# Performance work log

Measured on AMD Instinct MI355X. Metric: run time of the kernel, lower is better.

The kernel has to match this reference:

```python
import jax, jax.numpy as jnp
import numpy as np

DIM = 128
N_VARS = 2048
N_CLAUSES = 8192
N_ROUNDS = 26
ADJ_DENSITY = 0.0015  # ~6 literals per clause


def setup_inputs() -> dict:
    key = jax.random.key(0)
    ks = iter(jax.random.split(key, 40))

    def w(shape):
        fan_in = shape[-1]
        return jax.random.normal(next(ks), shape, jnp.float32) / jnp.sqrt(jnp.float32(fan_in))

    def b(shape):
        return jax.random.normal(next(ks), shape, jnp.float32) * 0.05

    adj = (jax.random.uniform(next(ks), (2 * N_VARS, N_CLAUSES)) < ADJ_DENSITY).astype(jnp.float32)
    inp = {
        'adj': adj,
        'l_init_w': w((DIM, 1)), 'l_init_b': b((DIM,)),
        'c_init_w': w((DIM, 1)), 'c_init_b': b((DIM,)),
        'lmsg_w1': w((DIM, DIM)), 'lmsg_b1': b((DIM,)),
        'lmsg_w2': w((DIM, DIM)), 'lmsg_b2': b((DIM,)),
        'lmsg_w3': w((DIM, DIM)), 'lmsg_b3': b((DIM,)),
        'cmsg_w1': w((DIM, DIM)), 'cmsg_b1': b((DIM,)),
        'cmsg_w2': w((DIM, DIM)), 'cmsg_b2': b((DIM,)),
        'cmsg_w3': w((DIM, DIM)), 'cmsg_b3': b((DIM,)),
        'l_wih': w((4 * DIM, 2 * DIM)), 'l_whh': w((4 * DIM, DIM)),
        'l_bih': b((4 * DIM,)), 'l_bhh': b((4 * DIM,)),
        'c_wih': w((4 * DIM, DIM)), 'c_whh': w((4 * DIM, DIM)),
        'c_bih': b((4 * DIM,)), 'c_bhh': b((4 * DIM,)),
        'lvote_w1': w((DIM, DIM)), 'lvote_b1': b((DIM,)),
        'lvote_w2': w((DIM, DIM)), 'lvote_b2': b((DIM,)),
        'lvote_w3': w((1, DIM)), 'lvote_b3': b((1,)),
    }
    return inp


def _mlp(x, w1, b1, w2, b2, w3, b3):
    x = jax.nn.relu(x @ w1.T + b1)
    x = jax.nn.relu(x @ w2.T + b2)
    return x @ w3.T + b3


def _lstm_step(x, h, c, wih, whh, bih, bhh):
    # torch.nn.LSTM gate order: i, f, g, o
    g = x @ wih.T + h @ whh.T + bih + bhh
    i, f, gg, o = jnp.split(g, 4, axis=-1)
    c = jax.nn.sigmoid(f) * c + jax.nn.sigmoid(i) * jnp.tanh(gg)
    h = jax.nn.sigmoid(o) * jnp.tanh(c)
    return h, c


def reference(adj, l_init_w, l_init_b, c_init_w, c_init_b,
              lmsg_w1, lmsg_b1, lmsg_w2, lmsg_b2, lmsg_w3, lmsg_b3,
              cmsg_w1, cmsg_b1, cmsg_w2, cmsg_b2, cmsg_w3, cmsg_b3,
              l_wih, l_whh, l_bih, l_bhh,
              c_wih, c_whh, c_bih, c_bhh,
              lvote_w1, lvote_b1, lvote_w2, lvote_b2, lvote_w3, lvote_b3):
    n_lits, n_clauses = adj.shape
    n_vars = n_lits // 2
    dim = l_init_b.shape[0]

    # L_init / C_init: Linear(1,dim) applied to ones(1), tiled across rows
    Lh = jnp.broadcast_to(l_init_w[:, 0] + l_init_b, (n_lits, dim))
    Ch = jnp.broadcast_to(c_init_w[:, 0] + c_init_b, (n_clauses, dim))
    Lc = jnp.zeros((n_lits, dim), jnp.float32)
    Cc = jnp.zeros((n_clauses, dim), jnp.float32)

    def step(carry, _):
        Lh, Lc, Ch, Cc = carry
        L_pre = _mlp(Lh, lmsg_w1, lmsg_b1, lmsg_w2, lmsg_b2, lmsg_w3, lmsg_b3)
        LC_msg = adj.T @ L_pre                       # [n_clauses, dim]
        Ch, Cc = _lstm_step(LC_msg, Ch, Cc, c_wih, c_whh, c_bih, c_bhh)
        C_pre = _mlp(Ch, cmsg_w1, cmsg_b1, cmsg_w2, cmsg_b2, cmsg_w3, cmsg_b3)
        CL_msg = adj @ C_pre                         # [2*n_vars, dim]
        L_flip = jnp.concatenate([Lh[n_vars:], Lh[:n_vars]], axis=0)
        x = jnp.concatenate([CL_msg, L_flip], axis=1)  # [2*n_vars, 2*dim]
        Lh, Lc = _lstm_step(x, Lh, Lc, l_wih, l_whh, l_bih, l_bhh)
        return (Lh, Lc, Ch, Cc), None

    (Lh, Lc, Ch, Cc), _ = jax.lax.scan(step, (Lh, Lc, Ch, Cc), None, length=N_ROUNDS)

    logits = Lh
    vote = _mlp(logits, lvote_w1, lvote_b1, lvote_w2, lvote_b2, lvote_w3, lvote_b3)  # [2*n_vars, 1]
    vote_join = jnp.concatenate([vote[:n_vars], vote[n_vars:]], axis=1)  # [n_vars, 2]
    vote_mean = jnp.mean(vote_join)[None]  # single problem in batch -> [1]
    return vote_mean, vote, logits
```

## Files before the change

### kernel.cpp

```cpp
#include <hip/hip_runtime.h>
#include <math.h>

#define NL 4096
#define NV 2048
#define NC 8192
#define DIM 128
#define NG 512
#define NROUNDS 26

#define CSEG 32
#define CSEGLEN 128
#define CSEGCAP 12
#define LSEG 32
#define LSEGLEN 256
#define LSEGCAP 16
#define CCAP 32
#define LCAP 48

__device__ __forceinline__ float sigf(float x){ return 1.0f/(1.0f+expf(-x)); }

__global__ void k_transpose(const float* __restrict__ src, float* __restrict__ dst,
                            int R, int C){
  __shared__ float t[32][33];
  int cb = blockIdx.x*32, rb = blockIdx.y*32;
  int x = threadIdx.x, y = threadIdx.y;
  for (int i = y; i < 32; i += 8){
    int r = rb+i, c = cb+x;
    if (r < R && c < C) t[i][x] = src[(size_t)r*C + c];
  }
  __syncthreads();
  for (int i = y; i < 32; i += 8){
    int c = cb+i, r = rb+x;
    if (c < C && r < R) dst[(size_t)c*R + r] = t[x][i];
  }
}

__global__ void k_permq(const float* __restrict__ W, int K,
                        float* __restrict__ dst, int koff){
  int idx = blockIdx.x*blockDim.x + threadIdx.x;
  if (idx >= K*NG) return;
  int k = idx >> 9, j = idx & (NG-1);
  int g = j & 3, d = j >> 2;
  dst[(size_t)(koff+k)*NG + j] = W[(size_t)(g*DIM+d)*K + k];
}

__global__ void k_permb(const float* __restrict__ bih, const float* __restrict__ bhh,
                        float* __restrict__ bq){
  int j = blockIdx.x*blockDim.x + threadIdx.x;
  if (j >= NG) return;
  int g = j & 3, d = j >> 2;
  bq[j] = bih[g*DIM+d] + bhh[g*DIM+d];
}

__global__ void k_build_cseg(const float* __restrict__ adj,
                             int* __restrict__ scnt, int* __restrict__ slst){
  int idx = blockIdx.x*blockDim.x + threadIdx.x;
  int c = idx & (NC-1);
  int s = idx >> 13;
  if (s >= CSEG) return;
  int base = s*CSEGLEN;
  int* out = slst + ((size_t)c*CSEG + s)*CSEGCAP;
  int n = 0;
  for (int i = 0; i < CSEGLEN; ++i){
    float v = adj[(size_t)(base+i)*NC + c];
    if (v != 0.0f){ if (n < CSEGCAP) out[n] = base+i; ++n; }
  }
  scnt[c*CSEG+s] = n < CSEGCAP ? n : CSEGCAP;
}

__global__ void k_build_lseg(const float* __restrict__ adj,
                             int* __restrict__ scnt, int* __restrict__ slst){
  int gtid = blockIdx.x*blockDim.x + threadIdx.x;
  int wid  = gtid >> 6;
  int lane = threadIdx.x & 63;
  int l = wid >> 5;
  int s = wid & (LSEG-1);
  if (l >= NL) return;
  int base = s*LSEGLEN;
  int* out = slst + ((size_t)l*LSEG + s)*LSEGCAP;
  int n = 0;
  for (int it = 0; it < LSEGLEN/64; ++it){
    int c = base + it*64 + lane;
    float v = adj[(size_t)l*NC + c];
    unsigned long long m = __ballot(v != 0.0f);
    if (v != 0.0f){
      int pos = n + __popcll(m & ((1ull<<lane)-1ull));
      if (pos < LSEGCAP) out[pos] = c;
    }
    n += __popcll(m);
  }
  if (lane == 0) scnt[l*LSEG+s] = n < LSEGCAP ? n : LSEGCAP;
}

__global__ void k_merge_c(const int* __restrict__ scnt, const int* __restrict__ slst,
                          int* __restrict__ cnt, int* __restrict__ lst){
  int c = blockIdx.x*blockDim.x + threadIdx.x;
  if (c >= NC) return;
  int n = 0;
  for (int s = 0; s < CSEG; ++s){
    int m = scnt[c*CSEG+s];
    const int* in = slst + ((size_t)c*CSEG+s)*CSEGCAP;
    for (int t = 0; t < m; ++t){ if (n < CCAP) lst[(size_t)c*CCAP+n] = in[t]; ++n; }
  }
  cnt[c] = n < CCAP ? n : CCAP;
}

__global__ void k_merge_l(const int* __restrict__ scnt, const int* __restrict__ slst,
                          int* __restrict__ cnt, int* __restrict__ lst){
  int l = blockIdx.x*blockDim.x + threadIdx.x;
  if (l >= NL) return;
  int n = 0;
  for (int s = 0; s < LSEG; ++s){
    int m = scnt[l*LSEG+s];
    const int* in = slst + ((size_t)l*LSEG+s)*LSEGCAP;
    for (int t = 0; t < m; ++t){ if (n < LCAP) lst[(size_t)l*LCAP+n] = in[t]; ++n; }
  }
  cnt[l] = n < LCAP ? n : LCAP;
}

__global__ void k_init(const float* __restrict__ liw, const float* __restrict__ lib,
                       const float* __restrict__ ciw, const float* __restrict__ cib,
                       float* __restrict__ Lh, float* __restrict__ Lc,
                       float* __restrict__ Ch, float* __restrict__ Cc){
  int idx = blockIdx.x*blockDim.x + threadIdx.x;
  int d = idx & (DIM-1);
  if (idx < NL*DIM){ Lh[idx] = liw[d] + lib[d]; Lc[idx] = 0.0f; }
  if (idx < NC*DIM){ Ch[idx] = ciw[d] + cib[d]; Cc[idx] = 0.0f; }
}

template<int CAP>
__global__ __launch_bounds__(256)
void k_gather(const float* __restrict__ X,
              const int* __restrict__ cnt, const int* __restrict__ lst,
              float* __restrict__ out){
  int tid = threadIdx.x;
  int r = blockIdx.x*8 + (tid>>5);
  int q = tid & 31;
  float4 s = make_float4(0.f,0.f,0.f,0.f);
  int n = cnt[r];
  const int* ls = lst + (size_t)r*CAP;
  for (int e = 0; e < n; ++e){
    float4 u = *(const float4*)&X[(size_t)ls[e]*DIM + q*4];
    s.x += u.x; s.y += u.y; s.z += u.z; s.w += u.w;
  }
  *(float4*)&out[(size_t)r*DIM + q*4] = s;
}

template<int ASRC, int BN>
__global__ __launch_bounds__(256)
void k_lstm(const float* __restrict__ Xmsg,
            const float* __restrict__ Hin,
            const float* __restrict__ Wq, const float* __restrict__ bq,
            float* __restrict__ Cst, float* __restrict__ Hout){
  constexpr int KT  = (ASRC==1) ? 256 : 384;
  constexpr int NT  = KT/16;
  constexpr int TN  = BN/16;
  constexpr int BQ  = BN/4;
  constexpr int NBS = (16*BQ)/256;
  __shared__ __align__(16) float As[16][68];
  __shared__ __align__(16) float4 Bs4[16*BQ];
  int tid = threadIdx.x;
  int tx = tid & 15, ty = tid >> 4;
  int m0 = blockIdx.x*64, n0 = blockIdx.y*BN;
  int arow = tid >> 2, akq = tid & 3;
  int grow = m0 + arow;
  int frow = (grow + NV) & (NL-1);

  float acc[4][TN];
#pragma unroll
  for (int r = 0; r < 4; ++r)
#pragma unroll
    for (int c = 0; c < TN; ++c) acc[r][c] = 0.f;

  for (int t = 0; t < NT; ++t){
    int k0 = t*16;
    const float* ap;
    if (ASRC == 1){
      ap = (k0 < 128) ? &Xmsg[(size_t)grow*DIM + k0]
                      : &Hin[(size_t)grow*DIM + (k0-128)];
    } else {
      ap = (k0 < 128) ? &Xmsg[(size_t)grow*DIM + k0]
         : (k0 < 256) ? &Hin[(size_t)frow*DIM + (k0-128)]
                      : &Hin[(size_t)grow*DIM + (k0-256)];
    }
    float4 av = *(const float4*)(ap + akq*4);
    float4 bv[NBS];
#pragma unroll
    for (int i = 0; i < NBS; ++i){
      int s = tid + i*256;
      int bk = s / BQ, bc = s % BQ;
      bv[i] = *(const float4*)&Wq[(size_t)(k0+bk)*NG + n0 + bc*4];
    }
    __syncthreads();
    As[akq*4+0][arow] = av.x;
    As[akq*4+1][arow] = av.y;
    As[akq*4+2][arow] = av.z;
    As[akq*4+3][arow] = av.w;
#pragma unroll
    for (int i = 0; i < NBS; ++i){
      int s = tid + i*256;
      int bk = s / BQ, bc = s % BQ;
      if (BN == 128) Bs4[(bk*2 + (bc&1))*16 + (bc>>1)] = bv[i];
      else           Bs4[bk*16 + bc] = bv[i];
    }
    __syncthreads();
#pragma unroll
    for (int k = 0; k < 16; ++k){
      float4 a = *(const float4*)&As[k][ty*4];
      float ar[4] = {a.x, a.y, a.z, a.w};
      if (TN == 8){
        float4 b0 = Bs4[(k*2+0)*16 + tx];
        float4 b1 = Bs4[(k*2+1)*16 + tx];
        float br[8] = {b0.x,b0.y,b0.z,b0.w,b1.x,b1.y,b1.z,b1.w};
#pragma unroll
        for (int r = 0; r < 4; ++r)
#pragma unroll
          for (int c = 0; c < 8; ++c) acc[r][c] += ar[r]*br[c];
      } else {
        float4 b0 = Bs4[k*16 + tx];
        float br[4] = {b0.x,b0.y,b0.z,b0.w};
#pragma unroll
        for (int r = 0; r < 4; ++r)
#pragma unroll
          for (int c = 0; c < 4; ++c) acc[r][c] += ar[r]*br[c];
      }
    }
  }

  if (TN == 8){
    float4 bq0 = *(const float4*)&bq[n0 + tx*8];
    float4 bq1 = *(const float4*)&bq[n0 + tx*8 + 4];
    int d0 = (n0 >> 2) + tx*2;
#pragma unroll
    for (int rr = 0; rr < 4; ++rr){
      int row = m0 + ty*4 + rr;
      float2 c = *(const float2*)&Cst[(size_t)row*DIM + d0];
      float i0 = acc[rr][0]+bq0.x, f0 = acc[rr][1]+bq0.y;
      float g0 = acc[rr][2]+bq0.z, o0 = acc[rr][3]+bq0.w;
      float i1 = acc[rr][4]+bq1.x, f1 = acc[rr][5]+bq1.y;
      float g1 = acc[rr][6]+bq1.z, o1 = acc[rr][7]+bq1.w;
      float cn0 = sigf(f0)*c.x + sigf(i0)*tanhf(g0);
      float cn1 = sigf(f1)*c.y + sigf(i1)*tanhf(g1);
      float hn0 = sigf(o0)*tanhf(cn0);
      float hn1 = sigf(o1)*tanhf(cn1);
      *(float2*)&Cst[(size_t)row*DIM + d0]  = make_float2(cn0, cn1);
      *(float2*)&Hout[(size_t)row*DIM + d0] = make_float2(hn0, hn1);
    }
  } else {
    float4 bqv = *(const float4*)&bq[n0 + tx*4];
    int d = (n0 >> 2) + tx;
#pragma unroll
    for (int rr = 0; rr < 4; ++rr){
      int row = m0 + ty*4 + rr;
      float c = Cst[(size_t)row*DIM + d];
      float ig = acc[rr][0]+bqv.x, fg = acc[rr][1]+bqv.y;
      float gg = acc[rr][2]+bqv.z, og = acc[rr][3]+bqv.w;
      float cn = sigf(fg)*c + sigf(ig)*tanhf(gg);
      float hn = sigf(og)*tanhf(cn);
      Cst[(size_t)row*DIM + d]  = cn;
      Hout[(size_t)row*DIM + d] = hn;
    }
  }
}

template<int BM>
__global__ __launch_bounds__(256)
void k_mlp3r(const float* __restrict__ in, float* __restrict__ out,
             const float* __restrict__ w1, const float* __restrict__ b1,
             const float* __restrict__ w2, const float* __restrict__ b2,
             const float* __restrict__ w3, const float* __restrict__ b3){
  constexpr int TM = BM/8;
  __shared__ __align__(16) float xs[BM][132];
  __shared__ __align__(16) float4 Bs4[512];
  int tid = threadIdx.x;
  int tx = tid & 31, ty = tid >> 5;
  int m0 = blockIdx.x*BM;
#pragma unroll
  for (int i = 0; i < BM/8; ++i){
    int idx = tid + i*256;
    int row = idx >> 5, c4 = idx & 31;
    *(float4*)&xs[row][c4*4] = *(const float4*)&in[(size_t)(m0+row)*DIM + c4*4];
  }
  const float* W[3] = {w1, w2, w3};
  const float* B[3] = {b1, b2, b3};
#pragma unroll
  for (int l = 0; l < 3; ++l){
    float acc[TM][4];
#pragma unroll
    for (int r = 0; r < TM; ++r)
#pragma unroll
      for (int c = 0; c < 4; ++c) acc[r][c] = 0.f;
    for (int kt = 0; kt < 8; ++kt){
      float4 wv0, wv1;
      { int s = tid;      wv0 = *(const float4*)&W[l][(size_t)(kt*16+(s>>5))*DIM + (s&31)*4]; }
      { int s = tid+256;  wv1 = *(const float4*)&W[l][(size_t)(kt*16+(s>>5))*DIM + (s&31)*4]; }
      __syncthreads();
      { int s = tid;      Bs4[(s>>5)*32 + (s&31)] = wv0; }
      { int s = tid+256;  Bs4[(s>>5)*32 + (s&31)] = wv1; }
      __syncthreads();
#pragma unroll
      for (int k4 = 0; k4 < 4; ++k4){
        float4 a[TM];
#pragma unroll
        for (int r = 0; r < TM; ++r)
          a[r] = *(const float4*)&xs[ty*TM+r][kt*16 + k4*4];
#pragma unroll
        for (int kk = 0; kk < 4; ++kk){
          float4 b = Bs4[(k4*4+kk)*32 + tx];
          float br[4] = {b.x, b.y, b.z, b.w};
#pragma unroll
          for (int r = 0; r < TM; ++r){
            float av = (kk==0) ? a[r].x : (kk==1) ? a[r].y : (kk==2) ? a[r].z : a[r].w;
#pragma unroll
            for (int c = 0; c < 4; ++c) acc[r][c] += av*br[c];
          }
        }
      }
    }
    float4 bb = *(const float4*)&B[l][tx*4];
    if (l < 2){
      __syncthreads();
#pragma unroll
      for (int r = 0; r < TM; ++r){
        float4 v = make_float4(fmaxf(acc[r][0]+bb.x, 0.f), fmaxf(acc[r][1]+bb.y, 0.f),
                               fmaxf(acc[r][2]+bb.z, 0.f), fmaxf(acc[r][3]+bb.w, 0.f));
        *(float4*)&xs[ty*TM+r][tx*4] = v;
      }
    } else {
#pragma unroll
      for (int r = 0; r < TM; ++r){
        int row = m0 + ty*TM + r;
        float4 v = make_float4(acc[r][0]+bb.x, acc[r][1]+bb.y,
                               acc[r][2]+bb.z, acc[r][3]+bb.w);
        *(float4*)&out[(size_t)row*DIM + tx*4] = v;
      }
    }
  }
}

template<bool RELU>
__device__ __forceinline__ void mlp_layer8v(const float (*__restrict__ xs)[DIM],
                                            float (*__restrict__ ys)[DIM],
                                            const float* __restrict__ Wt,
                                            const float* __restrict__ B, int tid){
  int j4 = (tid & 31)*4, slot = tid >> 5;
  float a0=0.f, a1=0.f, a2=0.f, a3=0.f;
#pragma unroll 4
  for (int k = 0; k < DIM; k += 4){
    float4 w0 = *(const float4*)&Wt[(size_t)(k+0)*DIM + j4];
    float4 w1 = *(const float4*)&Wt[(size_t)(k+1)*DIM + j4];
    float4 w2 = *(const float4*)&Wt[(size_t)(k+2)*DIM + j4];
    float4 w3 = *(const float4*)&Wt[(size_t)(k+3)*DIM + j4];
    float4 x  = *(const float4*)&xs[slot][k];
    a0 += x.x*w0.x + x.y*w1.x + x.z*w2.x + x.w*w3.x;
    a1 += x.x*w0.y + x.y*w1.y + x.z*w2.y + x.w*w3.y;
    a2 += x.x*w0.z + x.y*w1.z + x.z*w2.z + x.w*w3.z;
    a3 += x.x*w0.w + x.y*w1.w + x.z*w2.w + x.w*w3.w;
  }
  float4 b = *(const float4*)&B[j4];
  float4 v = make_float4(a0+b.x, a1+b.y, a2+b.z, a3+b.w);
  if (RELU){
    v.x = fmaxf(v.x,0.f); v.y = fmaxf(v.y,0.f);
    v.z = fmaxf(v.z,0.f); v.w = fmaxf(v.w,0.f);
  }
  *(float4*)&ys[slot][j4] = v;
}

__global__ __launch_bounds__(256, 4)
void k_vote(const float* __restrict__ Lh, float* __restrict__ vote,
            float* __restrict__ dout,
            const float* __restrict__ w1t, const float* __restrict__ b1,
            const float* __restrict__ w2t, const float* __restrict__ b2,
            const float* __restrict__ w3, const float* __restrict__ b3){
  __shared__ __align__(16) float xs[8][DIM];
  __shared__ __align__(16) float ys[8][DIM];
  int r0 = blockIdx.x*8;
  int tid = threadIdx.x;
  {
    int row = tid >> 5, c4 = (tid & 31)*4;
    float4 v = *(const float4*)&Lh[(size_t)(r0+row)*DIM + c4];
    *(float4*)&xs[row][c4] = v;
    *(float4*)&dout[1 + NL + (size_t)(r0+row)*DIM + c4] = v;
  }
  __syncthreads();
  mlp_layer8v<true>(xs, ys, w1t, b1, tid);
  __syncthreads();
  mlp_layer8v<true>(ys, xs, w2t, b2, tid);
  __syncthreads();
  int r = tid >> 5, lane32 = tid & 31;
  float4 x = *(const float4*)&xs[r][lane32*4];
  float4 w = *(const float4*)&w3[lane32*4];
  float pp = x.x*w.x + x.y*w.y + x.z*w.z + x.w*w.w;
  pp += __shfl_down(pp, 16, 32);
  pp += __shfl_down(pp, 8, 32);
  pp += __shfl_down(pp, 4, 32);
  pp += __shfl_down(pp, 2, 32);
  pp += __shfl_down(pp, 1, 32);
  if (lane32 == 0){
    float t = pp + b3[0];
    vote[r0+r] = t;
    dout[1 + r0 + r] = t;
  }
}

__global__ void k_mean(const float* __restrict__ vote, float* __restrict__ dout){
  __shared__ float red[256];
  int tid = threadIdx.x;
  float s = 0.f;
  for (int i = tid; i < NL; i += 256) s += vote[i];
  red[tid] = s;
  __syncthreads();
  for (int w = 128; w > 0; w >>= 1){
    if (tid < w) red[tid] += red[tid+w];
    __syncthreads();
  }
  if (tid == 0) dout[0] = red[0] / (float)NL;
}

static inline void launch_transpose(const float* src, float* dst, int R, int C,
                                    hipStream_t stream){
  dim3 g((C+31)/32, (R+31)/32), b(32, 8);
  k_transpose<<<g, b, 0, stream>>>(src, dst, R, C);
}

extern "C" void kernel_launch(void* const* d_in, const int* in_sizes, int n_in,
                              void* d_out, int out_size, void* d_ws, size_t ws_size,
                              hipStream_t stream){
  const float* adj      = (const float*)d_in[0];
  const float* l_init_w = (const float*)d_in[1];
  const float* l_init_b = (const float*)d_in[2];
  const float* c_init_w = (const float*)d_in[3];
  const float* c_init_b = (const float*)d_in[4];
  const float* lmsg_w1  = (const float*)d_in[5];
  const float* lmsg_b1  = (const float*)d_in[6];
  const float* lmsg_w2  = (const float*)d_in[7];
  const float* lmsg_b2  = (const float*)d_in[8];
  const float* lmsg_w3  = (const float*)d_in[9];
  const float* lmsg_b3  = (const float*)d_in[10];
  const float* cmsg_w1  = (const float*)d_in[11];
  const float* cmsg_b1  = (const float*)d_in[12];
  const float* cmsg_w2  = (const float*)d_in[13];
  const float* cmsg_b2  = (const float*)d_in[14];
  const float* cmsg_w3  = (const float*)d_in[15];
  const float* cmsg_b3  = (const float*)d_in[16];
  const float* l_wih    = (const float*)d_in[17];
  const float* l_whh    = (const float*)d_in[18];
  const float* l_bih    = (const float*)d_in[19];
  const float* l_bhh    = (const float*)d_in[20];
  const float* c_wih    = (const float*)d_in[21];
  const float* c_whh    = (const float*)d_in[22];
  const float* c_bih    = (const float*)d_in[23];
  const float* c_bhh    = (const float*)d_in[24];
  const float* lvote_w1 = (const float*)d_in[25];
  const float* lvote_b1 = (const float*)d_in[26];
  const float* lvote_w2 = (const float*)d_in[27];
  const float* lvote_b2 = (const float*)d_in[28];
  const float* lvote_w3 = (const float*)d_in[29];
  const float* lvote_b3 = (const float*)d_in[30];

  char* p = (char*)d_ws;
  auto alloc = [&](size_t bytes) -> void* {
    void* r = (void*)p;
    p += (bytes + 255) & ~(size_t)255;
    return r;
  };
  float* LhA   = (float*)alloc((size_t)NL*DIM*4);
  float* LhB   = (float*)alloc((size_t)NL*DIM*4);
  float* Lc    = (float*)alloc((size_t)NL*DIM*4);
  float* ChA   = (float*)alloc((size_t)NC*DIM*4);
  float* Cc    = (float*)alloc((size_t)NC*DIM*4);
  float* vote  = (float*)alloc((size_t)NL*4);
  int* ccnt    = (int*)alloc((size_t)NC*4);
  int* clst    = (int*)alloc((size_t)NC*CCAP*4);
  int* lcnt    = (int*)alloc((size_t)NL*4);
  int* llst    = (int*)alloc((size_t)NL*LCAP*4);
  float* lm1t  = (float*)alloc((size_t)DIM*DIM*4);
  float* lm2t  = (float*)alloc((size_t)DIM*DIM*4);
  float* lm3t  = (float*)alloc((size_t)DIM*DIM*4);
  float* cm1t  = (float*)alloc((size_t)DIM*DIM*4);
  float* cm2t  = (float*)alloc((size_t)DIM*DIM*4);
  float* cm3t  = (float*)alloc((size_t)DIM*DIM*4);
  float* vw1t  = (float*)alloc((size_t)DIM*DIM*4);
  float* vw2t  = (float*)alloc((size_t)DIM*DIM*4);
  float* WqC   = (float*)alloc((size_t)256*NG*4);
  float* WqL   = (float*)alloc((size_t)384*NG*4);
  float* bqC   = (float*)alloc((size_t)NG*4);
  float* bqL   = (float*)alloc((size_t)NG*4);
  char* scratch = (char*)alloc((size_t)24*1024*1024);
  int* scnt_c  = (int*)scratch;
  int* slst_c  = (int*)(scratch + (size_t)NC*CSEG*4);
  int* scnt_l  = (int*)(scratch + (size_t)(NC*CSEG + NC*CSEG*CSEGCAP)*4);
  int* slst_l  = (int*)(scratch + (size_t)(NC*CSEG + NC*CSEG*CSEGCAP + NL*LSEG)*4);
  float* ChB   = (float*)(scratch);
  float* Cpre  = (float*)(scratch + (size_t)4*1024*1024);
  float* Lpre  = (float*)(scratch + (size_t)8*1024*1024);
  float* Cmsg  = (float*)(scratch + (size_t)10*1024*1024);
  float* Lmsg  = (float*)(scratch + (size_t)14*1024*1024);
  (void)ws_size; (void)in_sizes; (void)n_in; (void)out_size;

  launch_transpose(lmsg_w1, lm1t, DIM, DIM, stream);
  launch_transpose(lmsg_w2, lm2t, DIM, DIM, stream);
  launch_transpose(lmsg_w3, lm3t, DIM, DIM, stream);
  launch_transpose(cmsg_w1, cm1t, DIM, DIM, stream);
  launch_transpose(cmsg_w2, cm2t, DIM, DIM, stream);
  launch_transpose(cmsg_w3, cm3t, DIM, DIM, stream);
  launch_transpose(lvote_w1, vw1t, DIM, DIM, stream);
  launch_transpose(lvote_w2, vw2t, DIM, DIM, stream);
  k_permq<<<(128*NG)/256, 256, 0, stream>>>(c_wih, 128, WqC, 0);
  k_permq<<<(128*NG)/256, 256, 0, stream>>>(c_whh, 128, WqC, 128);
  k_permq<<<(256*NG)/256, 256, 0, stream>>>(l_wih, 256, WqL, 0);
  k_permq<<<(128*NG)/256, 256, 0, stream>>>(l_whh, 128, WqL, 256);
  k_permb<<<NG/256, 256, 0, stream>>>(c_bih, c_bhh, bqC);
  k_permb<<<NG/256, 256, 0, stream>>>(l_bih, l_bhh, bqL);

  k_build_cseg<<<NC*CSEG/256, 256, 0, stream>>>(adj, scnt_c, slst_c);
  k_build_lseg<<<NL*LSEG*64/256, 256, 0, stream>>>(adj, scnt_l, slst_l);
  k_merge_c<<<NC/256, 256, 0, stream>>>(scnt_c, slst_c, ccnt, clst);
  k_merge_l<<<NL/256, 256, 0, stream>>>(scnt_l, slst_l, lcnt, llst);
  k_init<<<NC*DIM/256, 256, 0, stream>>>(l_init_w, l_init_b, c_init_w, c_init_b,
                                         LhA, Lc, ChA, Cc);

  float* Lh_cur = LhA; float* Lh_nxt = LhB;
  float* Ch_cur = ChA; float* Ch_nxt = ChB;

  k_mlp3r<8><<<NL/8, 256, 0, stream>>>(Lh_cur, Lpre,
                                       lm1t, lmsg_b1, lm2t, lmsg_b2, lm3t, lmsg_b3);
  for (int r = 0; r < NROUNDS; ++r){
    k_gather<CCAP><<<NC/8, 256, 0, stream>>>(Lpre, ccnt, clst, Cmsg);
    k_lstm<1,128><<<dim3(NC/64, 4), 256, 0, stream>>>(Cmsg, Ch_cur, WqC, bqC, Cc, Ch_nxt);
    k_mlp3r<16><<<NC/16, 256, 0, stream>>>(Ch_nxt, Cpre,
                                           cm1t, cmsg_b1, cm2t, cmsg_b2, cm3t, cmsg_b3);
    k_gather<LCAP><<<NL/8, 256, 0, stream>>>(Cpre, lcnt, llst, Lmsg);
    k_lstm<2,64><<<dim3(NL/64, 8), 256, 0, stream>>>(Lmsg, Lh_cur, WqL, bqL, Lc, Lh_nxt);
    k_mlp3r<8><<<NL/8, 256, 0, stream>>>(Lh_nxt, Lpre,
                                         lm1t, lmsg_b1, lm2t, lmsg_b2, lm3t, lmsg_b3);
    float* t;
    t = Lh_cur; Lh_cur = Lh_nxt; Lh_nxt = t;
    t = Ch_cur; Ch_cur = Ch_nxt; Ch_nxt = t;
  }

  k_vote<<<NL/8, 256, 0, stream>>>(Lh_cur, vote, (float*)d_out,
                                   vw1t, lvote_b1, vw2t, lvote_b2,
                                   lvote_w3, lvote_b3);
  k_mean<<<1, 256, 0, stream>>>(vote, (float*)d_out);
}
```

Measured before the change: 3.620 ms.

## Fuse sparse neighbor gather into LSTM GEMM A-tile loads

Removes the standalone k_gather kernels and the Cmsg/Lmsg intermediate buffers. The LSTM GEMM now builds the message part of its A tile on the fly by summing neighbor rows via the adjacency lists. This saves two launches per round and a write/read of the message tensors. In exchange, every column block in the grid repeats the gather (4x for clauses, 8x for literals), and serial dependent loads now sit inside the k-loop before a barrier.

```diff
diff --git a/kernel.cpp b/kernel.cpp
--- a/kernel.cpp
+++ b/kernel.cpp
@@ -128,27 +128,10 @@
   if (idx < NC*DIM){ Ch[idx] = ciw[d] + cib[d]; Cc[idx] = 0.0f; }
 }
 
-template<int CAP>
-__global__ __launch_bounds__(256)
-void k_gather(const float* __restrict__ X,
-              const int* __restrict__ cnt, const int* __restrict__ lst,
-              float* __restrict__ out){
-  int tid = threadIdx.x;
-  int r = blockIdx.x*8 + (tid>>5);
-  int q = tid & 31;
-  float4 s = make_float4(0.f,0.f,0.f,0.f);
-  int n = cnt[r];
-  const int* ls = lst + (size_t)r*CAP;
-  for (int e = 0; e < n; ++e){
-    float4 u = *(const float4*)&X[(size_t)ls[e]*DIM + q*4];
-    s.x += u.x; s.y += u.y; s.z += u.z; s.w += u.w;
-  }
-  *(float4*)&out[(size_t)r*DIM + q*4] = s;
-}
-
 template<int ASRC, int BN>
 __global__ __launch_bounds__(256)
-void k_lstm(const float* __restrict__ Xmsg,
+void k_lstm(const float* __restrict__ Xg,
+            const int* __restrict__ cnt, const int* __restrict__ lst,
             const float* __restrict__ Hin,
             const float* __restrict__ Wq, const float* __restrict__ bq,
             float* __restrict__ Cst, float* __restrict__ Hout){
@@ -157,6 +140,7 @@
   constexpr int TN  = BN/16;
   constexpr int BQ  = BN/4;
   constexpr int NBS = (16*BQ)/256;
+  constexpr int LCP = (ASRC==1) ? CCAP : LCAP;
   __shared__ __align__(16) float As[16][68];
   __shared__ __align__(16) float4 Bs4[16*BQ];
   int tid = threadIdx.x;
@@ -165,6 +149,8 @@
   int arow = tid >> 2, akq = tid & 3;
   int grow = m0 + arow;
   int frow = (grow + NV) & (NL-1);
+  int gn = cnt[grow];
+  const int* gls = lst + (size_t)grow*LCP;
 
   float acc[4][TN];
 #pragma unroll
@@ -174,16 +160,20 @@
 
   for (int t = 0; t < NT; ++t){
     int k0 = t*16;
-    const float* ap;
-    if (ASRC == 1){
-      ap = (k0 < 128) ? &Xmsg[(size_t)grow*DIM + k0]
-                      : &Hin[(size_t)grow*DIM + (k0-128)];
+    float4 av;
+    if (k0 < 128){
+      av = make_float4(0.f, 0.f, 0.f, 0.f);
+      for (int e = 0; e < gn; ++e){
+        float4 u = *(const float4*)&Xg[(size_t)gls[e]*DIM + k0 + akq*4];
+        av.x += u.x; av.y += u.y; av.z += u.z; av.w += u.w;
+      }
+    } else if (ASRC == 1){
+      av = *(const float4*)&Hin[(size_t)grow*DIM + (k0-128) + akq*4];
+    } else if (k0 < 256){
+      av = *(const float4*)&Hin[(size_t)frow*DIM + (k0-128) + akq*4];
     } else {
-      ap = (k0 < 128) ? &Xmsg[(size_t)grow*DIM + k0]
-         : (k0 < 256) ? &Hin[(size_t)frow*DIM + (k0-128)]
-                      : &Hin[(size_t)grow*DIM + (k0-256)];
-    }
-    float4 av = *(const float4*)(ap + akq*4);
+      av = *(const float4*)&Hin[(size_t)grow*DIM + (k0-256) + akq*4];
+    }
     float4 bv[NBS];
 #pragma unroll
     for (int i = 0; i < NBS; ++i){
@@ -494,8 +484,6 @@
   float* ChB   = (float*)(scratch);
   float* Cpre  = (float*)(scratch + (size_t)4*1024*1024);
   float* Lpre  = (float*)(scratch + (size_t)8*1024*1024);
-  float* Cmsg  = (float*)(scratch + (size_t)10*1024*1024);
-  float* Lmsg  = (float*)(scratch + (size_t)14*1024*1024);
   (void)ws_size; (void)in_sizes; (void)n_in; (void)out_size;
 
   launch_transpose(lmsg_w1, lm1t, DIM, DIM, stream);
@@ -526,12 +514,12 @@
   k_mlp3r<8><<<NL/8, 256, 0, stream>>>(Lh_cur, Lpre,
                                        lm1t, lmsg_b1, lm2t, lmsg_b2, lm3t, lmsg_b3);
   for (int r = 0; r < NROUNDS; ++r){
-    k_gather<CCAP><<<NC/8, 256, 0, stream>>>(Lpre, ccnt, clst, Cmsg);
-    k_lstm<1,128><<<dim3(NC/64, 4), 256, 0, stream>>>(Cmsg, Ch_cur, WqC, bqC, Cc, Ch_nxt);
+    k_lstm<1,128><<<dim3(NC/64, 4), 256, 0, stream>>>(
+        Lpre, ccnt, clst, Ch_cur, WqC, bqC, Cc, Ch_nxt);
     k_mlp3r<16><<<NC/16, 256, 0, stream>>>(Ch_nxt, Cpre,
                                            cm1t, cmsg_b1, cm2t, cmsg_b2, cm3t, cmsg_b3);
-    k_gather<LCAP><<<NL/8, 256, 0, stream>>>(Cpre, lcnt, llst, Lmsg);
-    k_lstm<2,64><<<dim3(NL/64, 8), 256, 0, stream>>>(Lmsg, Lh_cur, WqL, bqL, Lc, Lh_nxt);
+    k_lstm<2,64><<<dim3(NL/64, 8), 256, 0, stream>>>(
+        Cpre, lcnt, llst, Lh_cur, WqL, bqL, Lc, Lh_nxt);
     k_mlp3r<8><<<NL/8, 256, 0, stream>>>(Lh_nxt, Lpre,
                                          lm1t, lmsg_b1, lm2t, lmsg_b2, lm3t, lmsg_b3);
     float* t;
```

Result: slower. 5.239 ms (+44.7%).

## Fuse LSTM step with following message MLP into single kernel

Applied to the files above, without the earlier changes.

Combines the LSTM gate GEMM and cell update with the subsequent three-layer message MLP, keeping the new hidden state in shared memory instead of writing and rereading it. Each block now processes a small row tile (16 or 8 rows) across all 512 gate columns, removing one launch per side per round. The trade-off is far less reuse of the gate weight matrix per block, increasing weight reads from cache and lowering arithmetic intensity.

```diff
diff --git a/kernel.cpp b/kernel.cpp
--- a/kernel.cpp
+++ b/kernel.cpp
@@ -146,94 +146,101 @@
   *(float4*)&out[(size_t)r*DIM + q*4] = s;
 }
 
-template<int ASRC, int BN>
+template<int ASRC>
 __global__ __launch_bounds__(256)
-void k_lstm(const float* __restrict__ Xmsg,
-            const float* __restrict__ Hin,
-            const float* __restrict__ Wq, const float* __restrict__ bq,
-            float* __restrict__ Cst, float* __restrict__ Hout){
-  constexpr int KT  = (ASRC==1) ? 256 : 384;
-  constexpr int NT  = KT/16;
-  constexpr int TN  = BN/16;
-  constexpr int BQ  = BN/4;
-  constexpr int NBS = (16*BQ)/256;
-  __shared__ __align__(16) float As[16][68];
-  __shared__ __align__(16) float4 Bs4[16*BQ];
+void k_lstm_mlp(const float* __restrict__ Xmsg,
+                const float* __restrict__ Hin,
+                const float* __restrict__ Wq, const float* __restrict__ bq,
+                float* __restrict__ Cst, float* __restrict__ Hout,
+                const float* __restrict__ mw1, const float* __restrict__ mb1,
+                const float* __restrict__ mw2, const float* __restrict__ mb2,
+                const float* __restrict__ mw3, const float* __restrict__ mb3,
+                float* __restrict__ Pre){
+  constexpr int BM = (ASRC==1) ? 16 : 8;
+  constexpr int TM = (ASRC==1) ? 4  : 2;
+  constexpr int KT = (ASRC==1) ? 256 : 384;
+  constexpr int NT = KT/16;
+  __shared__ __align__(16) float As[16][BM+4];
+  __shared__ __align__(16) float4 Bs4[16*130];
+  __shared__ __align__(16) float xs[BM][132];
   int tid = threadIdx.x;
-  int tx = tid & 15, ty = tid >> 4;
-  int m0 = blockIdx.x*64, n0 = blockIdx.y*BN;
+  int tx = tid & 63, ty = tid >> 6;
+  int m0 = blockIdx.x*BM;
+
+  float acc[TM][8];
+#pragma unroll
+  for (int r = 0; r < TM; ++r)
+#pragma unroll
+    for (int c = 0; c < 8; ++c) acc[r][c] = 0.f;
+
+  bool aact = tid < BM*4;
   int arow = tid >> 2, akq = tid & 3;
   int grow = m0 + arow;
   int frow = (grow + NV) & (NL-1);
 
-  float acc[4][TN];
-#pragma unroll
-  for (int r = 0; r < 4; ++r)
-#pragma unroll
-    for (int c = 0; c < TN; ++c) acc[r][c] = 0.f;
-
   for (int t = 0; t < NT; ++t){
     int k0 = t*16;
-    const float* ap;
-    if (ASRC == 1){
-      ap = (k0 < 128) ? &Xmsg[(size_t)grow*DIM + k0]
-                      : &Hin[(size_t)grow*DIM + (k0-128)];
-    } else {
-      ap = (k0 < 128) ? &Xmsg[(size_t)grow*DIM + k0]
-         : (k0 < 256) ? &Hin[(size_t)frow*DIM + (k0-128)]
-                      : &Hin[(size_t)grow*DIM + (k0-256)];
-    }
-    float4 av = *(const float4*)(ap + akq*4);
-    float4 bv[NBS];
-#pragma unroll
-    for (int i = 0; i < NBS; ++i){
+    float4 av;
+    if (aact){
+      const float* ap;
+      if (ASRC == 1){
+        ap = (k0 < 128) ? &Xmsg[(size_t)grow*DIM + k0]
+                        : &Hin[(size_t)grow*DIM + (k0-128)];
+      } else {
+        ap = (k0 < 128) ? &Xmsg[(size_t)grow*DIM + k0]
+           : (k0 < 256) ? &Hin[(size_t)frow*DIM + (k0-128)]
+                        : &Hin[(size_t)grow*DIM + (k0-256)];
+      }
+      av = *(const float4*)(ap + akq*4);
+    }
+    float4 bv[8];
+#pragma unroll
+    for (int i = 0; i < 8; ++i){
       int s = tid + i*256;
-      int bk = s / BQ, bc = s % BQ;
-      bv[i] = *(const float4*)&Wq[(size_t)(k0+bk)*NG + n0 + bc*4];
+      int bk = s >> 7, bqd = s & 127;
+      bv[i] = *(const float4*)&Wq[(size_t)(k0+bk)*NG + bqd*4];
     }
     __syncthreads();
-    As[akq*4+0][arow] = av.x;
-    As[akq*4+1][arow] = av.y;
-    As[akq*4+2][arow] = av.z;
-    As[akq*4+3][arow] = av.w;
-#pragma unroll
-    for (int i = 0; i < NBS; ++i){
+    if (aact){
+      As[akq*4+0][arow] = av.x;
+      As[akq*4+1][arow] = av.y;
+      As[akq*4+2][arow] = av.z;
+      As[akq*4+3][arow] = av.w;
+    }
+#pragma unroll
+    for (int i = 0; i < 8; ++i){
       int s = tid + i*256;
-      int bk = s / BQ, bc = s % BQ;
-      if (BN == 128) Bs4[(bk*2 + (bc&1))*16 + (bc>>1)] = bv[i];
-      else           Bs4[bk*16 + bc] = bv[i];
+      int bk = s >> 7, bqd = s & 127;
+      Bs4[bk*130 + (bqd&1)*65 + (bqd>>1)] = bv[i];
     }
     __syncthreads();
 #pragma unroll
     for (int k = 0; k < 16; ++k){
-      float4 a = *(const float4*)&As[k][ty*4];
-      float ar[4] = {a.x, a.y, a.z, a.w};
-      if (TN == 8){
-        float4 b0 = Bs4[(k*2+0)*16 + tx];
-        float4 b1 = Bs4[(k*2+1)*16 + tx];
-        float br[8] = {b0.x,b0.y,b0.z,b0.w,b1.x,b1.y,b1.z,b1.w};
-#pragma unroll
-        for (int r = 0; r < 4; ++r)
-#pragma unroll
-          for (int c = 0; c < 8; ++c) acc[r][c] += ar[r]*br[c];
+      float ar[TM];
+      if (TM == 4){
+        float4 a = *(const float4*)&As[k][ty*4];
+        ar[0]=a.x; ar[1]=a.y; ar[2]=a.z; ar[3]=a.w;
       } else {
-        float4 b0 = Bs4[k*16 + tx];
-        float br[4] = {b0.x,b0.y,b0.z,b0.w};
-#pragma unroll
-        for (int r = 0; r < 4; ++r)
-#pragma unroll
-          for (int c = 0; c < 4; ++c) acc[r][c] += ar[r]*br[c];
-      }
-    }
-  }
-
-  if (TN == 8){
-    float4 bq0 = *(const float4*)&bq[n0 + tx*8];
-    float4 bq1 = *(const float4*)&bq[n0 + tx*8 + 4];
-    int d0 = (n0 >> 2) + tx*2;
-#pragma unroll
-    for (int rr = 0; rr < 4; ++rr){
-      int row = m0 + ty*4 + rr;
+        float2 a = *(const float2*)&As[k][ty*2];
+        ar[0]=a.x; ar[1]=a.y;
+      }
+      float4 b0 = Bs4[k*130 + tx];
+      float4 b1 = Bs4[k*130 + 65 + tx];
+      float br[8] = {b0.x,b0.y,b0.z,b0.w,b1.x,b1.y,b1.z,b1.w};
+#pragma unroll
+      for (int r = 0; r < TM; ++r)
+#pragma unroll
+        for (int c = 0; c < 8; ++c) acc[r][c] += ar[r]*br[c];
+    }
+  }
+
+  {
+    float4 bq0 = *(const float4*)&bq[tx*8];
+    float4 bq1 = *(const float4*)&bq[tx*8 + 4];
+    int d0 = tx*2;
+#pragma unroll
+    for (int rr = 0; rr < TM; ++rr){
+      int row = m0 + ty*TM + rr;
       float2 c = *(const float2*)&Cst[(size_t)row*DIM + d0];
       float i0 = acc[rr][0]+bq0.x, f0 = acc[rr][1]+bq0.y;
       float g0 = acc[rr][2]+bq0.z, o0 = acc[rr][3]+bq0.w;
@@ -245,20 +252,66 @@
       float hn1 = sigf(o1)*tanhf(cn1);
       *(float2*)&Cst[(size_t)row*DIM + d0]  = make_float2(cn0, cn1);
       *(float2*)&Hout[(size_t)row*DIM + d0] = make_float2(hn0, hn1);
-    }
-  } else {
-    float4 bqv = *(const float4*)&bq[n0 + tx*4];
-    int d = (n0 >> 2) + tx;
-#pragma unroll
-    for (int rr = 0; rr < 4; ++rr){
-      int row = m0 + ty*4 + rr;
-      float c = Cst[(size_t)row*DIM + d];
-      float ig = acc[rr][0]+bqv.x, fg = acc[rr][1]+bqv.y;
-      float gg = acc[rr][2]+bqv.z, og = acc[rr][3]+bqv.w;
-      float cn = sigf(fg)*c + sigf(ig)*tanhf(gg);
-      float hn = sigf(og)*tanhf(cn);
-      Cst[(size_t)row*DIM + d]  = cn;
-      Hout[(size_t)row*DIM + d] = hn;
+      *(float2*)&xs[ty*TM + rr][d0] = make_float2(hn0, hn1);
+    }
+  }
+  __syncthreads();
+
+  constexpr int TM2 = BM/8;
+  int tx2 = tid & 31, ty2 = tid >> 5;
+  const float* W[3] = {mw1, mw2, mw3};
+  const float* B[3] = {mb1, mb2, mb3};
+#pragma unroll
+  for (int l = 0; l < 3; ++l){
+    float macc[TM2][4];
+#pragma unroll
+    for (int r = 0; r < TM2; ++r)
+#pragma unroll
+      for (int c = 0; c < 4; ++c) macc[r][c] = 0.f;
+    for (int kt = 0; kt < 8; ++kt){
+      float4 wv0, wv1;
+      { int s = tid;      wv0 = *(const float4*)&W[l][(size_t)(kt*16+(s>>5))*DIM + (s&31)*4]; }
+      { int s = tid+256;  wv1 = *(const float4*)&W[l][(size_t)(kt*16+(s>>5))*DIM + (s&31)*4]; }
+      __syncthreads();
+      { int s = tid;      Bs4[(s>>5)*32 + (s&31)] = wv0; }
+      { int s = tid+256;  Bs4[(s>>5)*32 + (s&31)] = wv1; }
+      __syncthreads();
+#pragma unroll
+      for (int k4 = 0; k4 < 4; ++k4){
+        float4 a[TM2];
+#pragma unroll
+        for (int r = 0; r < TM2; ++r)
+          a[r] = *(const float4*)&xs[ty2*TM2+r][kt*16 + k4*4];
+#pragma unroll
+        for (int kk = 0; kk < 4; ++kk){
+          float4 b = Bs4[(k4*4+kk)*32 + tx2];
+          float br[4] = {b.x, b.y, b.z, b.w};
+#pragma unroll
+          for (int r = 0; r < TM2; ++r){
+            float av = (kk==0) ? a[r].x : (kk==1) ? a[r].y : (kk==2) ? a[r].z : a[r].w;
+#pragma unroll
+            for (int c = 0; c < 4; ++c) macc[r][c] += av*br[c];
+          }
+        }
+      }
+    }
+    float4 bb = *(const float4*)&B[l][tx2*4];
+    if (l < 2){
+      __syncthreads();
+#pragma unroll
+      for (int r = 0; r < TM2; ++r){
+        float4 v = make_float4(fmaxf(macc[r][0]+bb.x, 0.f), fmaxf(macc[r][1]+bb.y, 0.f),
+                               fmaxf(macc[r][2]+bb.z, 0.f), fmaxf(macc[r][3]+bb.w, 0.f));
+        *(float4*)&xs[ty2*TM2+r][tx2*4] = v;
+      }
+    } else {
+#pragma unroll
+      for (int r = 0; r < TM2; ++r){
+        int row = m0 + ty2*TM2 + r;
+        float4 v = make_float4(macc[r][0]+bb.x, macc[r][1]+bb.y,
+                               macc[r][2]+bb.z, macc[r][3]+bb.w);
+        *(float4*)&Pre[(size_t)row*DIM + tx2*4] = v;
+      }
     }
   }
 }
@@ -527,13 +580,13 @@
                                        lm1t, lmsg_b1, lm2t, lmsg_b2, lm3t, lmsg_b3);
   for (int r = 0; r < NROUNDS; ++r){
     k_gather<CCAP><<<NC/8, 256, 0, stream>>>(Lpre, ccnt, clst, Cmsg);
-    k_lstm<1,128><<<dim3(NC/64, 4), 256, 0, stream>>>(Cmsg, Ch_cur, WqC, bqC, Cc, Ch_nxt);
-    k_mlp3r<16><<<NC/16, 256, 0, stream>>>(Ch_nxt, Cpre,
-                                           cm1t, cmsg_b1, cm2t, cmsg_b2, cm3t, cmsg_b3);
+    k_lstm_mlp<1><<<NC/16, 256, 0, stream>>>(
+        Cmsg, Ch_cur, WqC, bqC, Cc, Ch_nxt,
+        cm1t, cmsg_b1, cm2t, cmsg_b2, cm3t, cmsg_b3, Cpre);
     k_gather<LCAP><<<NL/8, 256, 0, stream>>>(Cpre, lcnt, llst, Lmsg);
-    k_lstm<2,64><<<dim3(NL/64, 8), 256, 0, stream>>>(Lmsg, Lh_cur, WqL, bqL, Lc, Lh_nxt);
-    k_mlp3r<8><<<NL/8, 256, 0, stream>>>(Lh_nxt, Lpre,
-                                         lm1t, lmsg_b1, lm2t, lmsg_b2, lm3t, lmsg_b3);
+    k_lstm_mlp<2><<<NL/8, 256, 0, stream>>>(
+        Lmsg, Lh_cur, WqL, bqL, Lc, Lh_nxt,
+        lm1t, lmsg_b1, lm2t, lmsg_b2, lm3t, lmsg_b3, Lpre);
     float* t;
     t = Lh_cur; Lh_cur = Lh_nxt; Lh_nxt = t;
     t = Ch_cur; Ch_cur = Ch_nxt; Ch_nxt = t;
```

Result: slower. 6.774 ms (+87.1%).
